# Performance work log

Hardware: AMD Instinct MI355X
Metric: run time of the kernel (lower is better)

## Reference

```python
import jax, jax.numpy as jnp
import numpy as np

FFT_LEN = 512
HOP_LEN = 256
N_BLOCK = 4
N_BIN = FFT_LEN // 2 + 1  # 257
STATE_FACTOR = 0.99999
ALPHA_E = 0.7
BETA_F = 0.1
BATCH = 4096
N_MIC = 1


def setup_inputs() -> dict:
    key = jax.random.key(0)
    ks = jax.random.split(key, 7)
    return {
        "mic": jax.random.normal(ks[0], (BATCH, HOP_LEN, N_MIC), jnp.float32),
        "loudspeaker_buffer": jax.random.normal(ks[1], (BATCH, (N_BLOCK + 1) * HOP_LEN), jnp.float32),
        "phi_e": jax.random.uniform(ks[2], (BATCH, N_BIN, N_MIC), jnp.float32),
        "phi_f": jax.random.uniform(ks[3], (BATCH, N_BIN, N_BLOCK, N_MIC), jnp.float32),
        "P1": jax.random.uniform(ks[4], (BATCH, N_BIN, N_BLOCK, N_MIC), jnp.float32),
        "H_post_real": 0.1 * jax.random.normal(ks[5], (BATCH, N_BIN, N_BLOCK, N_MIC), jnp.float32),
        "H_post_imag": 0.1 * jax.random.normal(ks[6], (BATCH, N_BIN, N_BLOCK, N_MIC), jnp.float32),
    }


def reference(mic, loudspeaker_buffer, phi_e, phi_f, P1, H_post_real, H_post_imag):
    B = mic.shape[0]
    sf2 = STATE_FACTOR * STATE_FACTOR
    H_post = jax.lax.complex(H_post_real, H_post_imag)  # [B, n_bin, n_block, n_mic]

    # STFT of loudspeaker buffer: rectangular window, center=False -> n_block frames
    frame_idx = jnp.arange(N_BLOCK)[:, None] * HOP_LEN + jnp.arange(FFT_LEN)[None, :]
    frames = loudspeaker_buffer[:, frame_idx]              # [B, n_block, fft_len]
    X = jnp.swapaxes(jnp.fft.rfft(frames, axis=-1), 1, 2)  # [B, n_bin, n_block]

    # zero-padded rFFT of mic frame
    zpad = jnp.zeros((B, FFT_LEN - HOP_LEN, N_MIC), mic.dtype)
    fd_mic = jnp.fft.rfft(jnp.concatenate([zpad, mic], axis=1), n=FFT_LEN, axis=1)  # [B, n_bin, n_mic]

    H_prior = H_post
    # a-priori feedback estimate
    fd_fb_hat = jnp.sum(X[..., None] * H_prior, axis=2)                     # [B, n_bin, n_mic]
    est_fb = jnp.fft.irfft(fd_fb_hat, FFT_LEN, axis=1)[:, HOP_LEN:, :]      # [B, hop, n_mic]
    fd_est_fb = jnp.fft.rfft(jnp.concatenate([zpad, est_fb], axis=1), n=FFT_LEN, axis=1)
    E = fd_mic - fd_est_fb                                                  # [B, n_bin, n_mic]

    phi_e = ALPHA_E * phi_e + (1.0 - ALPHA_E) * jnp.abs(E) ** 2

    # Kalman gain
    phi_f = BETA_F * phi_f + (1.0 - BETA_F) * jnp.abs(H_prior) ** 2
    phi_n = (1.0 - sf2) * phi_f
    Xr = jnp.abs(X) ** 2                                                    # [B, n_bin, n_block]
    U = Xr[..., None] * P1                                                  # [B, n_bin, n_block, n_mic]
    R = U + 2.0 * phi_e[:, :, None, :] + 1e-10
    K = P1 * jnp.conj(X)[..., None] / R                                     # [B, n_bin, n_block, n_mic]
    P0 = jax.lax.stop_gradient(P1) - 0.5 * jax.lax.stop_gradient(jnp.abs(K) ** 2 * R)
    P1_new = sf2 * P0 + phi_n  # state update (not part of returned output)

    # filter update via gradient-constrained overlap-save
    dH = jnp.fft.irfft(K * E[:, :, None, :], FFT_LEN, axis=1)               # [B, fft_len, n_block, n_mic]
    mask = (jnp.arange(FFT_LEN) < HOP_LEN).astype(dH.dtype)[None, :, None, None]
    fd_dH = jnp.fft.rfft(dH * mask, n=FFT_LEN, axis=1)                      # [B, n_bin, n_block, n_mic]
    H_post_new = STATE_FACTOR * (H_prior + fd_dH)

    # a-posteriori feedback estimate and enhanced frame
    fd_fb_hat2 = jnp.sum(X[..., None] * H_post_new, axis=2)
    est_fb2 = jnp.fft.irfft(fd_fb_hat2, FFT_LEN, axis=1)[:, HOP_LEN:, :]
    enhanced = mic - est_fb2                                                # [B, hop, n_mic]
    return enhanced
```

## Files before the change

### kernel.cpp

```cpp
#include <hip/hip_runtime.h>
#include <math.h>

#define SF 0.99999f
#define PI2 6.283185307179586476925f
#define SWZ(c) ((c) ^ (((c) >> 4) & 15))
#define LDSFENCE() asm volatile("" ::: "memory")

template<int SGN>
__device__ __forceinline__ void twmul(float& ur, float& ui, float c, float s) {
    const float ss = (SGN < 0) ? -s : s;
    const float r = ur * c - ui * ss;
    const float i = ui * c + ur * ss;
    ur = r; ui = i;
}

template<int SGN>
__device__ __forceinline__ void bfly8(float* ur, float* ui) {
    const float C2 = 0.70710678118654752440f;
    float ar[4], ai[4], br[4], bi[4];
#pragma unroll
    for (int m = 0; m < 4; ++m) {
        ar[m] = ur[m] + ur[m + 4]; ai[m] = ui[m] + ui[m + 4];
        br[m] = ur[m] - ur[m + 4]; bi[m] = ui[m] - ui[m + 4];
    }
    float b1r, b1i, b2r, b2i, b3r, b3i;
    if (SGN < 0) {
        b1r = C2 * (br[1] + bi[1]); b1i = C2 * (bi[1] - br[1]);
        b2r = bi[2];                b2i = -br[2];
        b3r = C2 * (bi[3] - br[3]); b3i = -C2 * (br[3] + bi[3]);
    } else {
        b1r = C2 * (br[1] - bi[1]); b1i = C2 * (bi[1] + br[1]);
        b2r = -bi[2];               b2i = br[2];
        b3r = -C2 * (br[3] + bi[3]); b3i = C2 * (br[3] - bi[3]);
    }
    const float e0r = ar[0] + ar[2], e0i = ai[0] + ai[2];
    const float e1r = ar[0] - ar[2], e1i = ai[0] - ai[2];
    const float o0r = ar[1] + ar[3], o0i = ai[1] + ai[3];
    const float o1r = ar[1] - ar[3], o1i = ai[1] - ai[3];
    ur[0] = e0r + o0r; ui[0] = e0i + o0i;
    ur[4] = e0r - o0r; ui[4] = e0i - o0i;
    if (SGN < 0) { ur[2] = e1r + o1i; ui[2] = e1i - o1r; ur[6] = e1r - o1i; ui[6] = e1i + o1r; }
    else         { ur[2] = e1r - o1i; ui[2] = e1i + o1r; ur[6] = e1r + o1i; ui[6] = e1i - o1r; }
    const float f0r = br[0] + b2r, f0i = bi[0] + b2i;
    const float f1r = br[0] - b2r, f1i = bi[0] - b2i;
    const float g0r = b1r + b3r, g0i = b1i + b3i;
    const float g1r = b1r - b3r, g1i = b1i - b3i;
    ur[1] = f0r + g0r; ui[1] = f0i + g0i;
    ur[5] = f0r - g0r; ui[5] = f0i - g0i;
    if (SGN < 0) { ur[3] = f1r + g1i; ui[3] = f1i - g1r; ur[7] = f1r - g1i; ui[7] = f1i + g1r; }
    else         { ur[3] = f1r - g1i; ui[3] = f1i + g1r; ur[7] = f1r + g1i; ui[7] = f1i - g1r; }
}

template<int SGN>
__device__ __forceinline__ void fft512w(float* ur, float* ui,
                                        float2* __restrict__ buf,
                                        const float2* __restrict__ tw2,
                                        const float2* __restrict__ tw3,
                                        int t) {
    bfly8<SGN>(ur, ui);
    LDSFENCE();
#pragma unroll
    for (int m = 0; m < 8; ++m) buf[SWZ(8 * t + m)] = make_float2(ur[m], ui[m]);
    LDSFENCE();
#pragma unroll
    for (int m = 0; m < 8; ++m) { const float2 v = buf[SWZ(t + 64 * m)]; ur[m] = v.x; ui[m] = v.y; }
    const int k2 = t & 7;
#pragma unroll
    for (int m = 1; m < 8; ++m) { const float2 w = tw2[m * 8 + k2]; twmul<SGN>(ur[m], ui[m], w.x, w.y); }
    bfly8<SGN>(ur, ui);
    const int jj = ((t >> 3) << 6) + k2;
    LDSFENCE();
#pragma unroll
    for (int m = 0; m < 8; ++m) buf[SWZ(jj + 8 * m)] = make_float2(ur[m], ui[m]);
    LDSFENCE();
#pragma unroll
    for (int m = 0; m < 8; ++m) { const float2 v = buf[SWZ(t + 64 * m)]; ur[m] = v.x; ui[m] = v.y; }
#pragma unroll
    for (int m = 1; m < 8; ++m) { const float2 w = tw3[m * 64 + t]; twmul<SGN>(ur[m], ui[m], w.x, w.y); }
    bfly8<SGN>(ur, ui);
    LDSFENCE();
}

__global__ __launch_bounds__(256, 2) void pbfd_kernel(
    const float* __restrict__ g_mic,
    const float* __restrict__ g_lsb,
    const float* __restrict__ g_phie,
    const float* __restrict__ g_p1,
    const float* __restrict__ g_hr,
    const float* __restrict__ g_hi,
    float* __restrict__ g_out,
    int B) {
    __shared__ float2 tw2[64];
    __shared__ float2 tw3[512];
    __shared__ float2 xch[4][512];

    const int tid = threadIdx.x;
    for (int e = tid; e < 512; e += 256) {
        const int m = e >> 6, tt = e & 63;
        float s, c;
        sincosf(PI2 * (float)(m * tt) * (1.0f / 512.0f), &s, &c);
        tw3[e] = make_float2(c, s);
    }
    if (tid < 64) {
        const int m = tid >> 3, k = tid & 7;
        float s, c;
        sincosf(PI2 * (float)(m * k) * (1.0f / 64.0f), &s, &c);
        tw2[tid] = make_float2(c, s);
    }
    __syncthreads();

    const int w = tid >> 6;
    const int t = tid & 63;
    const int elem = blockIdx.x * 4 + w;
    if (elem >= B) return;
    float2* buf = &xch[w][0];
    const int ml = (64 - t) & 63;

    float mv[4];
    {
        const float* mp = g_mic + (size_t)elem * 256;
#pragma unroll
        for (int q = 0; q < 4; ++q) mv[q] = mp[t + 64 * q];
    }

    float xr[4][4], xi[4][4], xn[4];
    {
        const float* lb = g_lsb + (size_t)elem * 1280;
#pragma unroll
        for (int pr = 0; pr < 2; ++pr) {
            float ur[8], ui[8];
#pragma unroll
            for (int m = 0; m < 8; ++m) {
                ur[m] = lb[(2 * pr) * 256 + t + 64 * m];
                ui[m] = lb[(2 * pr + 1) * 256 + t + 64 * m];
            }
            fft512w<-1>(ur, ui, buf, tw2, tw3, t);
#pragma unroll
            for (int m = 0; m < 4; ++m) {
                float zmr = __shfl(ur[7 - m], ml);
                float zmi = __shfl(ui[7 - m], ml);
                if (t == 0) {
                    zmr = (m == 0) ? ur[0] : ur[8 - m];
                    zmi = (m == 0) ? ui[0] : ui[8 - m];
                }
                xr[2 * pr][m]     = 0.5f * (ur[m] + zmr);
                xi[2 * pr][m]     = 0.5f * (ui[m] - zmi);
                xr[2 * pr + 1][m] = 0.5f * (ui[m] + zmi);
                xi[2 * pr + 1][m] = -0.5f * (ur[m] - zmr);
            }
            if (t == 0) { xn[2 * pr] = ur[4]; xn[2 * pr + 1] = ui[4]; }
        }
    }

    float hr_[4][4], hi_[4][4], hn[4];
    {
        const float4* hr4 = (const float4*)g_hr + (size_t)elem * 257;
        const float4* hi4 = (const float4*)g_hi + (size_t)elem * 257;
#pragma unroll
        for (int m = 0; m < 4; ++m) {
            const float4 a = hr4[t + 64 * m], b = hi4[t + 64 * m];
            hr_[0][m] = a.x; hr_[1][m] = a.y; hr_[2][m] = a.z; hr_[3][m] = a.w;
            hi_[0][m] = b.x; hi_[1][m] = b.y; hi_[2][m] = b.z; hi_[3][m] = b.w;
        }
    }
    float pn[4] = {0, 0, 0, 0};
    if (t == 0) {
        const float4* hr4 = (const float4*)g_hr + (size_t)elem * 257;
        const float4* p14 = (const float4*)g_p1 + (size_t)elem * 257;
        const float4 a = hr4[256], p = p14[256];
        hn[0] = a.x; hn[1] = a.y; hn[2] = a.z; hn[3] = a.w;
        pn[0] = p.x; pn[1] = p.y; pn[2] = p.z; pn[3] = p.w;
    }

    auto sum_ifft = [&](float o4[4]) {
        float ur[8], ui[8];
#pragma unroll
        for (int m = 0; m < 4; ++m) {
            float cr = 0.f, ci = 0.f;
#pragma unroll
            for (int j = 0; j < 4; ++j) {
                cr += xr[j][m] * hr_[j][m] - xi[j][m] * hi_[j][m];
                ci += xr[j][m] * hi_[j][m] + xi[j][m] * hr_[j][m];
            }
            ur[m] = cr; ui[m] = ci;
        }
#pragma unroll
        for (int m = 4; m < 8; ++m) {
            const float cr = __shfl(ur[7 - m], ml);
            const float ci = __shfl(ui[7 - m], ml);
            ur[m] = cr; ui[m] = -ci;
        }
        if (t == 0) {
            ur[5] = ur[3]; ui[5] = -ui[3];
            ur[6] = ur[2]; ui[6] = -ui[2];
            ur[7] = ur[1]; ui[7] = -ui[1];
            float cn = 0.f;
#pragma unroll
            for (int j = 0; j < 4; ++j) cn += xn[j] * hn[j];
            ur[4] = cn; ui[4] = 0.f;
        }
        fft512w<1>(ur, ui, buf, tw2, tw3, t);
#pragma unroll
        for (int q = 0; q < 4; ++q) o4[q] = ur[4 + q] * (1.0f / 512.0f);
    };

    float d4[4];
    {
        float o4[4];
        sum_ifft(o4);
#pragma unroll
        for (int q = 0; q < 4; ++q) d4[q] = mv[q] - o4[q];
    }

    float er[4], ei[4], en = 0.f;
    {
        float ur[8], ui[8];
#pragma unroll
        for (int m = 0; m < 4; ++m) { ur[m] = 0.f; ui[m] = 0.f; }
#pragma unroll
        for (int q = 0; q < 4; ++q) { ur[4 + q] = d4[q]; ui[4 + q] = 0.f; }
        fft512w<-1>(ur, ui, buf, tw2, tw3, t);
#pragma unroll
        for (int m = 0; m < 4; ++m) { er[m] = ur[m]; ei[m] = ui[m]; }
        if (t == 0) en = ur[4];
    }

    float pe[4], pen = 0.f;
    {
        const float* php = g_phie + (size_t)elem * 257;
#pragma unroll
        for (int m = 0; m < 4; ++m)
            pe[m] = 0.7f * php[t + 64 * m] + 0.3f * (er[m] * er[m] + ei[m] * ei[m]);
        if (t == 0) pen = 0.7f * php[256] + 0.3f * en * en;
    }

    {
        const float4* p14 = (const float4*)g_p1 + (size_t)elem * 257;
#pragma unroll
        for (int pr = 0; pr < 2; ++pr) {
            const int j0 = 2 * pr, j1 = 2 * pr + 1;
            float ur[8], ui[8], gr[4], gi[4];
#pragma unroll
            for (int m = 0; m < 4; ++m) {
                const float4 p = p14[t + 64 * m];
                const float pa = pr ? p.z : p.x;
                const float pb = pr ? p.w : p.y;
                const float xxa = xr[j0][m] * xr[j0][m] + xi[j0][m] * xi[j0][m];
                const float Ra = xxa * pa + 2.f * pe[m] + 1e-10f;
                const float ia = 1.f / Ra;
                const float kra = pa * xr[j0][m] * ia, kia = -pa * xi[j0][m] * ia;
                const float a_r = kra * er[m] - kia * ei[m];
                const float a_i = kra * ei[m] + kia * er[m];
                const float xxb = xr[j1][m] * xr[j1][m] + xi[j1][m] * xi[j1][m];
                const float Rb = xxb * pb + 2.f * pe[m] + 1e-10f;
                const float ib = 1.f / Rb;
                const float krb = pb * xr[j1][m] * ib, kib = -pb * xi[j1][m] * ib;
                const float b_r = krb * er[m] - kib * ei[m];
                const float b_i = krb * ei[m] + kib * er[m];
                ur[m] = a_r - b_i;  ui[m] = a_i + b_r;
                gr[m] = a_r + b_i;  gi[m] = b_r - a_i;
            }
#pragma unroll
            for (int m = 4; m < 8; ++m) {
                ur[m] = __shfl(gr[7 - m], ml);
                ui[m] = __shfl(gi[7 - m], ml);
            }
            if (t == 0) {
                ur[5] = gr[3]; ui[5] = gi[3];
                ur[6] = gr[2]; ui[6] = gi[2];
                ur[7] = gr[1]; ui[7] = gi[1];
                const float Rn0 = xn[j0] * xn[j0] * pn[j0] + 2.f * pen + 1e-10f;
                const float Rn1 = xn[j1] * xn[j1] * pn[j1] + 2.f * pen + 1e-10f;
                ur[4] = pn[j0] * xn[j0] / Rn0 * en;
                ui[4] = pn[j1] * xn[j1] / Rn1 * en;
            }
            fft512w<1>(ur, ui, buf, tw2, tw3, t);
#pragma unroll
            for (int m = 0; m < 4; ++m) { ur[m] *= (1.0f / 512.0f); ui[m] *= (1.0f / 512.0f); }
#pragma unroll
            for (int m = 4; m < 8; ++m) { ur[m] = 0.f; ui[m] = 0.f; }
            fft512w<-1>(ur, ui, buf, tw2, tw3, t);
#pragma unroll
            for (int m = 0; m < 4; ++m) {
                float zmr = __shfl(ur[7 - m], ml);
                float zmi = __shfl(ui[7 - m], ml);
                if (t == 0) {
                    zmr = (m == 0) ? ur[0] : ur[8 - m];
                    zmi = (m == 0) ? ui[0] : ui[8 - m];
                }
                const float f0r = 0.5f * (ur[m] + zmr), f0i = 0.5f * (ui[m] - zmi);
                const float f1r = 0.5f * (ui[m] + zmi), f1i = -0.5f * (ur[m] - zmr);
                hr_[j0][m] = SF * (hr_[j0][m] + f0r);
                hi_[j0][m] = SF * (hi_[j0][m] + f0i);
                hr_[j1][m] = SF * (hr_[j1][m] + f1r);
                hi_[j1][m] = SF * (hi_[j1][m] + f1i);
            }
            if (t == 0) {
                hn[j0] = SF * (hn[j0] + ur[4]);
                hn[j1] = SF * (hn[j1] + ui[4]);
            }
        }
    }

    {
        float o4[4];
        sum_ifft(o4);
        float* op = g_out + (size_t)elem * 256;
#pragma unroll
        for (int q = 0; q < 4; ++q) op[t + 64 * q] = mv[q] - o4[q];
    }
}

extern "C" void kernel_launch(void* const* d_in, const int* in_sizes, int n_in,
                              void* d_out, int out_size, void* d_ws, size_t ws_size,
                              hipStream_t stream) {
    const float* mic  = (const float*)d_in[0];
    const float* lsb  = (const float*)d_in[1];
    const float* phie = (const float*)d_in[2];
    const float* p1   = (const float*)d_in[4];
    const float* hr   = (const float*)d_in[5];
    const float* hi   = (const float*)d_in[6];
    float* out = (float*)d_out;

    const int B = in_sizes[0] / 256;
    const int blocks = (B + 3) / 4;
    pbfd_kernel<<<blocks, 256, 0, stream>>>(mic, lsb, phie, p1, hr, hi, out, B);
}
```

Measured before the change: 38.01 us.

## Hoist all global loads before twiddle setup and park Nyquist scalars in LDS

All per-element global inputs (loudspeaker buffer, H, mic, phi_e, P1 and the Nyquist entries) are now loaded into registers at kernel entry, before the twiddle-table sincos setup and barrier. This lets memory latency overlap with twiddle generation. Lane-0-only Nyquist scalars move into a small per-wave LDS array to free registers. Out-of-range elements are clamped instead of returning early, so the barrier stays uniform. The extra ~40 live registers risk spills or lower occupancy under launch_bounds(256,2).

```diff
diff --git a/kernel.cpp b/kernel.cpp
--- a/kernel.cpp
+++ b/kernel.cpp
@@ -93,8 +93,62 @@
     __shared__ float2 tw2[64];
     __shared__ float2 tw3[512];
     __shared__ float2 xch[4][512];
+    __shared__ float nyq[4][14];
 
     const int tid = threadIdx.x;
+    const int w = tid >> 6;
+    const int t = tid & 63;
+    const int elem = blockIdx.x * 4 + w;
+    const int ec = (elem < B) ? elem : (B - 1);
+    const int ml = (64 - t) & 63;
+
+    float u[20];
+    {
+        const float* lb = g_lsb + (size_t)ec * 1280;
+#pragma unroll
+        for (int m = 0; m < 20; ++m) u[m] = lb[t + 64 * m];
+    }
+    float hr_[4][4], hi_[4][4];
+    {
+        const float4* hr4 = (const float4*)g_hr + (size_t)ec * 257;
+        const float4* hi4 = (const float4*)g_hi + (size_t)ec * 257;
+#pragma unroll
+        for (int m = 0; m < 4; ++m) {
+            const float4 a = hr4[t + 64 * m];
+            hr_[0][m] = a.x; hr_[1][m] = a.y; hr_[2][m] = a.z; hr_[3][m] = a.w;
+        }
+#pragma unroll
+        for (int m = 0; m < 4; ++m) {
+            const float4 b = hi4[t + 64 * m];
+            hi_[0][m] = b.x; hi_[1][m] = b.y; hi_[2][m] = b.z; hi_[3][m] = b.w;
+        }
+    }
+    float mv[4];
+    {
+        const float* mp = g_mic + (size_t)ec * 256;
+#pragma unroll
+        for (int q = 0; q < 4; ++q) mv[q] = mp[t + 64 * q];
+    }
+    float phv[4];
+    {
+        const float* php = g_phie + (size_t)ec * 257;
+#pragma unroll
+        for (int m = 0; m < 4; ++m) phv[m] = php[t + 64 * m];
+    }
+    float4 p1q[4];
+    {
+        const float4* p14 = (const float4*)g_p1 + (size_t)ec * 257;
+#pragma unroll
+        for (int m = 0; m < 4; ++m) p1q[m] = p14[t + 64 * m];
+    }
+    float4 hnl = make_float4(0.f, 0.f, 0.f, 0.f), pnl = make_float4(0.f, 0.f, 0.f, 0.f);
+    float ph256 = 0.f;
+    if (t == 0) {
+        hnl = ((const float4*)g_hr)[(size_t)ec * 257 + 256];
+        pnl = ((const float4*)g_p1)[(size_t)ec * 257 + 256];
+        ph256 = g_phie[(size_t)ec * 257 + 256];
+    }
+
     for (int e = tid; e < 512; e += 256) {
         const int m = e >> 6, tt = e & 63;
         float s, c;
@@ -109,67 +163,37 @@
     }
     __syncthreads();
 
-    const int w = tid >> 6;
-    const int t = tid & 63;
-    const int elem = blockIdx.x * 4 + w;
-    if (elem >= B) return;
     float2* buf = &xch[w][0];
-    const int ml = (64 - t) & 63;
-
-    float mv[4];
-    {
-        const float* mp = g_mic + (size_t)elem * 256;
-#pragma unroll
-        for (int q = 0; q < 4; ++q) mv[q] = mp[t + 64 * q];
-    }
-
-    float xr[4][4], xi[4][4], xn[4];
-    {
-        const float* lb = g_lsb + (size_t)elem * 1280;
-#pragma unroll
-        for (int pr = 0; pr < 2; ++pr) {
-            float ur[8], ui[8];
-#pragma unroll
-            for (int m = 0; m < 8; ++m) {
-                ur[m] = lb[(2 * pr) * 256 + t + 64 * m];
-                ui[m] = lb[(2 * pr + 1) * 256 + t + 64 * m];
+    float* ny = &nyq[w][0];
+    if (t == 0) {
+        ny[4] = hnl.x; ny[5] = hnl.y; ny[6] = hnl.z; ny[7] = hnl.w;
+        ny[8] = pnl.x; ny[9] = pnl.y; ny[10] = pnl.z; ny[11] = pnl.w;
+        ny[12] = ph256;
+    }
+    LDSFENCE();
+
+    float xr[4][4], xi[4][4];
+#pragma unroll
+    for (int pr = 0; pr < 2; ++pr) {
+        float ur[8], ui[8];
+#pragma unroll
+        for (int m = 0; m < 8; ++m) { ur[m] = u[8 * pr + m]; ui[m] = u[8 * pr + m + 4]; }
+        fft512w<-1>(ur, ui, buf, tw2, tw3, t);
+#pragma unroll
+        for (int m = 0; m < 4; ++m) {
+            float zmr = __shfl(ur[7 - m], ml);
+            float zmi = __shfl(ui[7 - m], ml);
+            if (t == 0) {
+                zmr = (m == 0) ? ur[0] : ur[8 - m];
+                zmi = (m == 0) ? ui[0] : ui[8 - m];
             }
-            fft512w<-1>(ur, ui, buf, tw2, tw3, t);
-#pragma unroll
-            for (int m = 0; m < 4; ++m) {
-                float zmr = __shfl(ur[7 - m], ml);
-                float zmi = __shfl(ui[7 - m], ml);
-                if (t == 0) {
-                    zmr = (m == 0) ? ur[0] : ur[8 - m];
-                    zmi = (m == 0) ? ui[0] : ui[8 - m];
-                }
-                xr[2 * pr][m]     = 0.5f * (ur[m] + zmr);
-                xi[2 * pr][m]     = 0.5f * (ui[m] - zmi);
-                xr[2 * pr + 1][m] = 0.5f * (ui[m] + zmi);
-                xi[2 * pr + 1][m] = -0.5f * (ur[m] - zmr);
-            }
-            if (t == 0) { xn[2 * pr] = ur[4]; xn[2 * pr + 1] = ui[4]; }
-        }
-    }
-
-    float hr_[4][4], hi_[4][4], hn[4];
-    {
-        const float4* hr4 = (const float4*)g_hr + (size_t)elem * 257;
-        const float4* hi4 = (const float4*)g_hi + (size_t)elem * 257;
-#pragma unroll
-        for (int m = 0; m < 4; ++m) {
-            const float4 a = hr4[t + 64 * m], b = hi4[t + 64 * m];
-            hr_[0][m] = a.x; hr_[1][m] = a.y; hr_[2][m] = a.z; hr_[3][m] = a.w;
-            hi_[0][m] = b.x; hi_[1][m] = b.y; hi_[2][m] = b.z; hi_[3][m] = b.w;
-        }
-    }
-    float pn[4] = {0, 0, 0, 0};
-    if (t == 0) {
-        const float4* hr4 = (const float4*)g_hr + (size_t)elem * 257;
-        const float4* p14 = (const float4*)g_p1 + (size_t)elem * 257;
-        const float4 a = hr4[256], p = p14[256];
-        hn[0] = a.x; hn[1] = a.y; hn[2] = a.z; hn[3] = a.w;
-        pn[0] = p.x; pn[1] = p.y; pn[2] = p.z; pn[3] = p.w;
+            xr[2 * pr][m]     = 0.5f * (ur[m] + zmr);
+            xi[2 * pr][m]     = 0.5f * (ui[m] - zmi);
+            xr[2 * pr + 1][m] = 0.5f * (ui[m] + zmi);
+            xi[2 * pr + 1][m] = -0.5f * (ur[m] - zmr);
+        }
+        if (t == 0) { ny[0 + 2 * pr] = ur[4]; ny[1 + 2 * pr] = ui[4]; }
+        LDSFENCE();
     }
 
     auto sum_ifft = [&](float o4[4]) {
@@ -196,7 +220,7 @@
             ur[7] = ur[1]; ui[7] = -ui[1];
             float cn = 0.f;
 #pragma unroll
-            for (int j = 0; j < 4; ++j) cn += xn[j] * hn[j];
+            for (int j = 0; j < 4; ++j) cn += ny[j] * ny[4 + j];
             ur[4] = cn; ui[4] = 0.f;
         }
         fft512w<1>(ur, ui, buf, tw2, tw3, t);
@@ -212,7 +236,7 @@
         for (int q = 0; q < 4; ++q) d4[q] = mv[q] - o4[q];
     }
 
-    float er[4], ei[4], en = 0.f;
+    float er[4], ei[4];
     {
         float ur[8], ui[8];
 #pragma unroll
@@ -222,92 +246,95 @@
         fft512w<-1>(ur, ui, buf, tw2, tw3, t);
 #pragma unroll
         for (int m = 0; m < 4; ++m) { er[m] = ur[m]; ei[m] = ui[m]; }
-        if (t == 0) en = ur[4];
-    }
-
-    float pe[4], pen = 0.f;
-    {
-        const float* php = g_phie + (size_t)elem * 257;
-#pragma unroll
-        for (int m = 0; m < 4; ++m)
-            pe[m] = 0.7f * php[t + 64 * m] + 0.3f * (er[m] * er[m] + ei[m] * ei[m]);
-        if (t == 0) pen = 0.7f * php[256] + 0.3f * en * en;
-    }
-
-    {
-        const float4* p14 = (const float4*)g_p1 + (size_t)elem * 257;
-#pragma unroll
-        for (int pr = 0; pr < 2; ++pr) {
-            const int j0 = 2 * pr, j1 = 2 * pr + 1;
-            float ur[8], ui[8], gr[4], gi[4];
-#pragma unroll
-            for (int m = 0; m < 4; ++m) {
-                const float4 p = p14[t + 64 * m];
-                const float pa = pr ? p.z : p.x;
-                const float pb = pr ? p.w : p.y;
-                const float xxa = xr[j0][m] * xr[j0][m] + xi[j0][m] * xi[j0][m];
-                const float Ra = xxa * pa + 2.f * pe[m] + 1e-10f;
-                const float ia = 1.f / Ra;
-                const float kra = pa * xr[j0][m] * ia, kia = -pa * xi[j0][m] * ia;
-                const float a_r = kra * er[m] - kia * ei[m];
-                const float a_i = kra * ei[m] + kia * er[m];
-                const float xxb = xr[j1][m] * xr[j1][m] + xi[j1][m] * xi[j1][m];
-                const float Rb = xxb * pb + 2.f * pe[m] + 1e-10f;
-                const float ib = 1.f / Rb;
-                const float krb = pb * xr[j1][m] * ib, kib = -pb * xi[j1][m] * ib;
-                const float b_r = krb * er[m] - kib * ei[m];
-                const float b_i = krb * ei[m] + kib * er[m];
-                ur[m] = a_r - b_i;  ui[m] = a_i + b_r;
-                gr[m] = a_r + b_i;  gi[m] = b_r - a_i;
+        if (t == 0) {
+            const float en = ur[4];
+            ny[13] = en;
+            ny[12] = 0.7f * ny[12] + 0.3f * en * en;
+        }
+        LDSFENCE();
+    }
+
+    float pe[4];
+#pragma unroll
+    for (int m = 0; m < 4; ++m)
+        pe[m] = 0.7f * phv[m] + 0.3f * (er[m] * er[m] + ei[m] * ei[m]);
+
+#pragma unroll
+    for (int pr = 0; pr < 2; ++pr) {
+        const int j0 = 2 * pr, j1 = 2 * pr + 1;
+        float ur[8], ui[8], gr[4], gi[4];
+#pragma unroll
+        for (int m = 0; m < 4; ++m) {
+            const float pa = pr ? p1q[m].z : p1q[m].x;
+            const float pb = pr ? p1q[m].w : p1q[m].y;
+            const float xxa = xr[j0][m] * xr[j0][m] + xi[j0][m] * xi[j0][m];
+            const float Ra = xxa * pa + 2.f * pe[m] + 1e-10f;
+            const float ia = 1.f / Ra;
+            const float kra = pa * xr[j0][m] * ia, kia = -pa * xi[j0][m] * ia;
+            const float a_r = kra * er[m] - kia * ei[m];
+            const float a_i = kra * ei[m] + kia * er[m];
+            const float xxb = xr[j1][m] * xr[j1][m] + xi[j1][m] * xi[j1][m];
+            const float Rb = xxb * pb + 2.f * pe[m] + 1e-10f;
+            const float ib = 1.f / Rb;
+            const float krb = pb * xr[j1][m] * ib, kib = -pb * xi[j1][m] * ib;
+            const float b_r = krb * er[m] - kib * ei[m];
+            const float b_i = krb * ei[m] + kib * er[m];
+            ur[m] = a_r - b_i;  ui[m] = a_i + b_r;
+            gr[m] = a_r + b_i;  gi[m] = b_r - a_i;
+        }
+#pragma unroll
+        for (int m = 4; m < 8; ++m) {
+            ur[m] = __shfl(gr[7 - m], ml);
+            ui[m] = __shfl(gi[7 - m], ml);
+        }
+        if (t == 0) {
+            ur[5] = gr[3]; ui[5] = gi[3];
+            ur[6] = gr[2]; ui[6] = gi[2];
+            ur[7] = gr[1]; ui[7] = gi[1];
+            const float xn0 = ny[j0], xn1 = ny[j1];
+            const float pn0 = ny[8 + j0], pn1 = ny[8 + j1];
+            const float en = ny[13], pen = ny[12];
+            const float Rn0 = xn0 * xn0 * pn0 + 2.f * pen + 1e-10f;
+            const float Rn1 = xn1 * xn1 * pn1 + 2.f * pen + 1e-10f;
+            ur[4] = pn0 * xn0 / Rn0 * en;
+            ui[4] = pn1 * xn1 / Rn1 * en;
+        }
+        fft512w<1>(ur, ui, buf, tw2, tw3, t);
+#pragma unroll
+        for (int m = 0; m < 4; ++m) { ur[m] *= (1.0f / 512.0f); ui[m] *= (1.0f / 512.0f); }
+#pragma unroll
+        for (int m = 4; m < 8; ++m) { ur[m] = 0.f; ui[m] = 0.f; }
+        fft512w<-1>(ur, ui, buf, tw2, tw3, t);
+#pragma unroll
+        for (int m = 0; m < 4; ++m) {
+            float zmr = __shfl(ur[7 - m], ml);
+            float zmi = __shfl(ui[7 - m], ml);
+            if (t == 0) {
+                zmr = (m == 0) ? ur[0] : ur[8 - m];
+                zmi = (m == 0) ? ui[0] : ui[8 - m];
             }
-#pragma unroll
-            for (int m = 4; m < 8; ++m) {
-                ur[m] = __shfl(gr[7 - m], ml);
-                ui[m] = __shfl(gi[7 - m], ml);
-            }
-            if (t == 0) {
-                ur[5] = gr[3]; ui[5] = gi[3];
-                ur[6] = gr[2]; ui[6] = gi[2];
-                ur[7] = gr[1]; ui[7] = gi[1];
-                const float Rn0 = xn[j0] * xn[j0] * pn[j0] + 2.f * pen + 1e-10f;
-                const float Rn1 = xn[j1] * xn[j1] * pn[j1] + 2.f * pen + 1e-10f;
-                ur[4] = pn[j0] * xn[j0] / Rn0 * en;
-                ui[4] = pn[j1] * xn[j1] / Rn1 * en;
-            }
-            fft512w<1>(ur, ui, buf, tw2, tw3, t);
-#pragma unroll
-            for (int m = 0; m < 4; ++m) { ur[m] *= (1.0f / 512.0f); ui[m] *= (1.0f / 512.0f); }
-#pragma unroll
-            for (int m = 4; m < 8; ++m) { ur[m] = 0.f; ui[m] = 0.f; }
-            fft512w<-1>(ur, ui, buf, tw2, tw3, t);
-#pragma unroll
-            for (int m = 0; m < 4; ++m) {
-                float zmr = __shfl(ur[7 - m], ml);
-                float zmi = __shfl(ui[7 - m], ml);
-                if (t == 0) {
-                    zmr = (m == 0) ? ur[0] : ur[8 - m];
-                    zmi = (m == 0) ? ui[0] : ui[8 - m];
-                }
-                const float f0r = 0.5f * (ur[m] + zmr), f0i = 0.5f * (ui[m] - zmi);
-                const float f1r = 0.5f * (ui[m] + zmi), f1i = -0.5f * (ur[m] - zmr);
-                hr_[j0][m] = SF * (hr_[j0][m] + f0r);
-                hi_[j0][m] = SF * (hi_[j0][m] + f0i);
-                hr_[j1][m] = SF * (hr_[j1][m] + f1r);
-                hi_[j1][m] = SF * (hi_[j1][m] + f1i);
-            }
-            if (t == 0) {
-                hn[j0] = SF * (hn[j0] + ur[4]);
-                hn[j1] = SF * (hn[j1] + ui[4]);
-            }
-        }
+            const float f0r = 0.5f * (ur[m] + zmr), f0i = 0.5f * (ui[m] - zmi);
+            const float f1r = 0.5f * (ui[m] + zmi), f1i = -0.5f * (ur[m] - zmr);
+            hr_[j0][m] = SF * (hr_[j0][m] + f0r);
+            hi_[j0][m] = SF * (hi_[j0][m] + f0i);
+            hr_[j1][m] = SF * (hr_[j1][m] + f1r);
+            hi_[j1][m] = SF * (hi_[j1][m] + f1i);
+        }
+        if (t == 0) {
+            ny[4 + j0] = SF * (ny[4 + j0] + ur[4]);
+            ny[4 + j1] = SF * (ny[4 + j1] + ui[4]);
+        }
+        LDSFENCE();
     }
 
     {
         float o4[4];
         sum_ifft(o4);
-        float* op = g_out + (size_t)elem * 256;
-#pragma unroll
-        for (int q = 0; q < 4; ++q) op[t + 64 * q] = mv[q] - o4[q];
+        if (elem < B) {
+            float* op = g_out + (size_t)elem * 256;
+#pragma unroll
+            for (int q = 0; q < 4; ++q) op[t + 64 * q] = mv[q] - o4[q];
+        }
     }
 }
 
```

Measured after the change: 40.37 us. 6.2% more time.

## Use linearity to reuse prior feedback estimate and drop H register state

Applied to the files above, without the earlier changes.

The final a-posteriori estimate is rewritten using linearity. SF*(H+dH) summed against X gives SF*(prior estimate + irfft of sum X*dH), so the kernel accumulates only the X-weighted update Dr/Di and reuses the already computed prior time-domain estimate. This lets the 32 H_post registers go out of scope after the first pass, which lowers register pressure and removes the per-block H update. The swizzled LDS read addresses are also precomputed once per thread into an array. The result changes slightly in floating point because of the reordered arithmetic.

```diff
diff --git a/kernel.cpp b/kernel.cpp
--- a/kernel.cpp
+++ b/kernel.cpp
@@ -56,14 +56,14 @@
                                         float2* __restrict__ buf,
                                         const float2* __restrict__ tw2,
                                         const float2* __restrict__ tw3,
-                                        int t) {
+                                        const int* ra, int t) {
     bfly8<SGN>(ur, ui);
     LDSFENCE();
 #pragma unroll
     for (int m = 0; m < 8; ++m) buf[SWZ(8 * t + m)] = make_float2(ur[m], ui[m]);
     LDSFENCE();
 #pragma unroll
-    for (int m = 0; m < 8; ++m) { const float2 v = buf[SWZ(t + 64 * m)]; ur[m] = v.x; ui[m] = v.y; }
+    for (int m = 0; m < 8; ++m) { const float2 v = buf[ra[m]]; ur[m] = v.x; ui[m] = v.y; }
     const int k2 = t & 7;
 #pragma unroll
     for (int m = 1; m < 8; ++m) { const float2 w = tw2[m * 8 + k2]; twmul<SGN>(ur[m], ui[m], w.x, w.y); }
@@ -74,7 +74,7 @@
     for (int m = 0; m < 8; ++m) buf[SWZ(jj + 8 * m)] = make_float2(ur[m], ui[m]);
     LDSFENCE();
 #pragma unroll
-    for (int m = 0; m < 8; ++m) { const float2 v = buf[SWZ(t + 64 * m)]; ur[m] = v.x; ui[m] = v.y; }
+    for (int m = 0; m < 8; ++m) { const float2 v = buf[ra[m]]; ur[m] = v.x; ui[m] = v.y; }
 #pragma unroll
     for (int m = 1; m < 8; ++m) { const float2 w = tw3[m * 64 + t]; twmul<SGN>(ur[m], ui[m], w.x, w.y); }
     bfly8<SGN>(ur, ui);
@@ -116,6 +116,10 @@
     float2* buf = &xch[w][0];
     const int ml = (64 - t) & 63;
 
+    int ra[8];
+#pragma unroll
+    for (int m = 0; m < 8; ++m) ra[m] = SWZ(t + 64 * m);
+
     float mv[4];
     {
         const float* mp = g_mic + (size_t)elem * 256;
@@ -134,7 +138,7 @@
                 ur[m] = lb[(2 * pr) * 256 + t + 64 * m];
                 ui[m] = lb[(2 * pr + 1) * 256 + t + 64 * m];
             }
-            fft512w<-1>(ur, ui, buf, tw2, tw3, t);
+            fft512w<-1>(ur, ui, buf, tw2, tw3, ra, t);
 #pragma unroll
             for (int m = 0; m < 4; ++m) {
                 float zmr = __shfl(ur[7 - m], ml);
@@ -152,80 +156,85 @@
         }
     }
 
-    float hr_[4][4], hi_[4][4], hn[4];
-    {
-        const float4* hr4 = (const float4*)g_hr + (size_t)elem * 257;
-        const float4* hi4 = (const float4*)g_hi + (size_t)elem * 257;
-#pragma unroll
-        for (int m = 0; m < 4; ++m) {
-            const float4 a = hr4[t + 64 * m], b = hi4[t + 64 * m];
-            hr_[0][m] = a.x; hr_[1][m] = a.y; hr_[2][m] = a.z; hr_[3][m] = a.w;
-            hi_[0][m] = b.x; hi_[1][m] = b.y; hi_[2][m] = b.z; hi_[3][m] = b.w;
-        }
-    }
-    float pn[4] = {0, 0, 0, 0};
-    if (t == 0) {
-        const float4* hr4 = (const float4*)g_hr + (size_t)elem * 257;
-        const float4* p14 = (const float4*)g_p1 + (size_t)elem * 257;
-        const float4 a = hr4[256], p = p14[256];
-        hn[0] = a.x; hn[1] = a.y; hn[2] = a.z; hn[3] = a.w;
-        pn[0] = p.x; pn[1] = p.y; pn[2] = p.z; pn[3] = p.w;
-    }
-
-    auto sum_ifft = [&](float o4[4]) {
+    auto herm_ifft = [&](const float cr[4], const float ci[4], float cn, float o4[4]) {
         float ur[8], ui[8];
 #pragma unroll
-        for (int m = 0; m < 4; ++m) {
-            float cr = 0.f, ci = 0.f;
-#pragma unroll
-            for (int j = 0; j < 4; ++j) {
-                cr += xr[j][m] * hr_[j][m] - xi[j][m] * hi_[j][m];
-                ci += xr[j][m] * hi_[j][m] + xi[j][m] * hr_[j][m];
-            }
-            ur[m] = cr; ui[m] = ci;
-        }
+        for (int m = 0; m < 4; ++m) { ur[m] = cr[m]; ui[m] = ci[m]; }
 #pragma unroll
         for (int m = 4; m < 8; ++m) {
-            const float cr = __shfl(ur[7 - m], ml);
-            const float ci = __shfl(ui[7 - m], ml);
-            ur[m] = cr; ui[m] = -ci;
+            ur[m] = __shfl(cr[7 - m], ml);
+            ui[m] = -__shfl(ci[7 - m], ml);
         }
         if (t == 0) {
-            ur[5] = ur[3]; ui[5] = -ui[3];
-            ur[6] = ur[2]; ui[6] = -ui[2];
-            ur[7] = ur[1]; ui[7] = -ui[1];
-            float cn = 0.f;
-#pragma unroll
-            for (int j = 0; j < 4; ++j) cn += xn[j] * hn[j];
+            ur[5] = cr[3]; ui[5] = -ci[3];
+            ur[6] = cr[2]; ui[6] = -ci[2];
+            ur[7] = cr[1]; ui[7] = -ci[1];
             ur[4] = cn; ui[4] = 0.f;
         }
-        fft512w<1>(ur, ui, buf, tw2, tw3, t);
+        fft512w<1>(ur, ui, buf, tw2, tw3, ra, t);
 #pragma unroll
         for (int q = 0; q < 4; ++q) o4[q] = ur[4 + q] * (1.0f / 512.0f);
     };
 
     float d4[4];
-    {
+    float pn[4], en = 0.f, pen = 0.f;
+    {
+        float hr_[4][4], hi_[4][4], hn[4];
+        {
+            const float4* hr4 = (const float4*)g_hr + (size_t)elem * 257;
+            const float4* hi4 = (const float4*)g_hi + (size_t)elem * 257;
+#pragma unroll
+            for (int m = 0; m < 4; ++m) {
+                const float4 a = hr4[t + 64 * m];
+                hr_[0][m] = a.x; hr_[1][m] = a.y; hr_[2][m] = a.z; hr_[3][m] = a.w;
+            }
+#pragma unroll
+            for (int m = 0; m < 4; ++m) {
+                const float4 b = hi4[t + 64 * m];
+                hi_[0][m] = b.x; hi_[1][m] = b.y; hi_[2][m] = b.z; hi_[3][m] = b.w;
+            }
+            if (t == 0) {
+                const float4 a = hr4[256];
+                const float4 p = ((const float4*)g_p1)[(size_t)elem * 257 + 256];
+                hn[0] = a.x; hn[1] = a.y; hn[2] = a.z; hn[3] = a.w;
+                pn[0] = p.x; pn[1] = p.y; pn[2] = p.z; pn[3] = p.w;
+            }
+        }
+        float cr[4], ci[4], cn = 0.f;
+#pragma unroll
+        for (int m = 0; m < 4; ++m) {
+            float sr = 0.f, si = 0.f;
+#pragma unroll
+            for (int j = 0; j < 4; ++j) {
+                sr += xr[j][m] * hr_[j][m] - xi[j][m] * hi_[j][m];
+                si += xr[j][m] * hi_[j][m] + xi[j][m] * hr_[j][m];
+            }
+            cr[m] = sr; ci[m] = si;
+        }
+        if (t == 0) {
+#pragma unroll
+            for (int j = 0; j < 4; ++j) cn += xn[j] * hn[j];
+        }
         float o4[4];
-        sum_ifft(o4);
+        herm_ifft(cr, ci, cn, o4);
 #pragma unroll
         for (int q = 0; q < 4; ++q) d4[q] = mv[q] - o4[q];
     }
 
-    float er[4], ei[4], en = 0.f;
+    float er[4], ei[4];
     {
         float ur[8], ui[8];
 #pragma unroll
         for (int m = 0; m < 4; ++m) { ur[m] = 0.f; ui[m] = 0.f; }
 #pragma unroll
         for (int q = 0; q < 4; ++q) { ur[4 + q] = d4[q]; ui[4 + q] = 0.f; }
-        fft512w<-1>(ur, ui, buf, tw2, tw3, t);
+        fft512w<-1>(ur, ui, buf, tw2, tw3, ra, t);
 #pragma unroll
         for (int m = 0; m < 4; ++m) { er[m] = ur[m]; ei[m] = ui[m]; }
         if (t == 0) en = ur[4];
     }
 
-    float pe[4], pen = 0.f;
+    float pe[4];
     {
         const float* php = g_phie + (size_t)elem * 257;
 #pragma unroll
@@ -234,6 +243,8 @@
         if (t == 0) pen = 0.7f * php[256] + 0.3f * en * en;
     }
 
+    float Dr[4] = {0, 0, 0, 0}, Di[4] = {0, 0, 0, 0};
+    float dn = 0.f;
     {
         const float4* p14 = (const float4*)g_p1 + (size_t)elem * 257;
 #pragma unroll
@@ -274,12 +285,12 @@
                 ur[4] = pn[j0] * xn[j0] / Rn0 * en;
                 ui[4] = pn[j1] * xn[j1] / Rn1 * en;
             }
-            fft512w<1>(ur, ui, buf, tw2, tw3, t);
+            fft512w<1>(ur, ui, buf, tw2, tw3, ra, t);
 #pragma unroll
             for (int m = 0; m < 4; ++m) { ur[m] *= (1.0f / 512.0f); ui[m] *= (1.0f / 512.0f); }
 #pragma unroll
             for (int m = 4; m < 8; ++m) { ur[m] = 0.f; ui[m] = 0.f; }
-            fft512w<-1>(ur, ui, buf, tw2, tw3, t);
+            fft512w<-1>(ur, ui, buf, tw2, tw3, ra, t);
 #pragma unroll
             for (int m = 0; m < 4; ++m) {
                 float zmr = __shfl(ur[7 - m], ml);
@@ -290,24 +301,20 @@
                 }
                 const float f0r = 0.5f * (ur[m] + zmr), f0i = 0.5f * (ui[m] - zmi);
                 const float f1r = 0.5f * (ui[m] + zmi), f1i = -0.5f * (ur[m] - zmr);
-                hr_[j0][m] = SF * (hr_[j0][m] + f0r);
-                hi_[j0][m] = SF * (hi_[j0][m] + f0i);
-                hr_[j1][m] = SF * (hr_[j1][m] + f1r);
-                hi_[j1][m] = SF * (hi_[j1][m] + f1i);
-            }
-            if (t == 0) {
-                hn[j0] = SF * (hn[j0] + ur[4]);
-                hn[j1] = SF * (hn[j1] + ui[4]);
-            }
+                Dr[m] += xr[j0][m] * f0r - xi[j0][m] * f0i + xr[j1][m] * f1r - xi[j1][m] * f1i;
+                Di[m] += xr[j0][m] * f0i + xi[j0][m] * f0r + xr[j1][m] * f1i + xi[j1][m] * f1r;
+            }
+            if (t == 0) dn += xn[j0] * ur[4] + xn[j1] * ui[4];
         }
     }
 
     {
         float o4[4];
-        sum_ifft(o4);
+        herm_ifft(Dr, Di, dn, o4);
         float* op = g_out + (size_t)elem * 256;
 #pragma unroll
-        for (int q = 0; q < 4; ++q) op[t + 64 * q] = mv[q] - o4[q];
+        for (int q = 0; q < 4; ++q)
+            op[t + 64 * q] = mv[q] - SF * ((mv[q] - d4[q]) + o4[q]);
     }
 }
 
```

New measurement: 36.76 us. -3.3%, faster.
